# Kernel optimization log

Measured on AMD Instinct MI355X. Metric: run time of the kernel, lower is better.

## Reference

```python
import jax, jax.numpy as jnp
import numpy as np

IN_FEATURES = 4096
OUT_FEATURES = 4096
BLOCK_SIZE = 64
P = 0.1          # fraction of blocks kept
N_TOKENS = 8192


def setup_inputs() -> dict:
    key = jax.random.key(0)
    k_x, k_w, k_m, k_b = jax.random.split(key, 4)
    x = jax.random.normal(k_x, (N_TOKENS, IN_FEATURES), dtype=jnp.float32)
    # kaiming_uniform_(a=sqrt(5)) on [out, in] -> bound = 1/sqrt(in_features)
    bound = 1.0 / np.sqrt(IN_FEATURES)
    weight = jax.random.uniform(k_w, (OUT_FEATURES, IN_FEATURES), dtype=jnp.float32,
                                minval=-bound, maxval=bound)
    bias = jax.random.uniform(k_b, (OUT_FEATURES,), dtype=jnp.float32,
                              minval=-bound, maxval=bound)
    # Block-structured 0/1 mask: keep each BLOCK_SIZE x BLOCK_SIZE block with prob P
    nb_out, nb_in = OUT_FEATURES // BLOCK_SIZE, IN_FEATURES // BLOCK_SIZE
    block_keep = (jax.random.uniform(k_m, (nb_out, nb_in)) < P).astype(jnp.float32)
    mask = jnp.repeat(jnp.repeat(block_keep, BLOCK_SIZE, axis=0), BLOCK_SIZE, axis=1)
    return {"input": x, "weight": weight, "bias": bias, "mask": mask}


def reference(input, weight, bias, mask):
    # bsr_dense_mm((W*mask).to_sparse_bsr(), x.T).T + bias == x @ (W*mask).T + bias
    masked_w = weight * mask                      # [out, in]
    return input @ masked_w.T + bias              # [N, out]
```

## Files before the change

### kernel.cpp

```cpp
#include <hip/hip_runtime.h>
#include <hip/hip_fp16.h>
#include <cstdint>

#define IN_F   4096
#define OUT_F  4096
#define BS     64
#define NB     64
#define N_TOK  8192
#define TM     256
#define NMT    (N_TOK / TM)

typedef __attribute__((ext_vector_type(8))) _Float16       f16x8;
typedef __attribute__((ext_vector_type(8))) unsigned short u16x8;
typedef __attribute__((ext_vector_type(4))) unsigned short u16x4;
typedef __attribute__((ext_vector_type(4))) float          f32x4;

#define WS_X16_OFF     0ull
#define WS_X16_BYTES   ((size_t)N_TOK * IN_F * 2ull)
#define WS_WT_OFF      (WS_X16_OFF + WS_X16_BYTES)
#define WS_WT_BYTES    (4096ull * 8192ull)
#define WS_NEEDED      (WS_WT_OFF + WS_WT_BYTES)

__device__ __forceinline__ unsigned long long mask_ballot(
        const float* __restrict__ mask, int br, int lane) {
    float mv = mask[(size_t)(br * BS) * IN_F + (size_t)lane * BS];
    return __ballot(mv != 0.0f);
}

__device__ __forceinline__ u16x8 pack8(f32x4 a, f32x4 b) {
    u16x8 o;
#pragma unroll
    for (int j = 0; j < 4; ++j) o[j]     = __half_as_ushort(__float2half_rn(a[j]));
#pragma unroll
    for (int j = 0; j < 4; ++j) o[4 + j] = __half_as_ushort(__float2half_rn(b[j]));
    return o;
}

__global__ __launch_bounds__(256)
void convert_all_kernel(const float* __restrict__ x,
                        const float* __restrict__ w,
                        const float* __restrict__ mask,
                        unsigned short* __restrict__ x16,
                        unsigned short* __restrict__ wt) {
    const int b = blockIdx.x;
    if (b < 4096) {
        const f32x4* xin = (const f32x4*)x;
        u16x4* xo = (u16x4*)x16;
        const size_t base = (size_t)b * 2048 + threadIdx.x;
#pragma unroll
        for (int it = 0; it < 8; ++it) {
            f32x4 v = xin[base + it * 256];
            u16x4 o;
#pragma unroll
            for (int j = 0; j < 4; ++j) o[j] = __half_as_ushort(__float2half_rn(v[j]));
            xo[base + it * 256] = o;
        }
    } else {
        const int wb   = b - 4096;
        const int br   = wb >> 6, si = wb & 63;
        const int lane = threadIdx.x & 63;
        unsigned long long ball = mask_ballot(mask, br, lane);
        if (si >= __popcll(ball)) return;
        bool fl = ((ball >> lane) & 1ull) &&
                  (__popcll(ball & ((1ull << lane) - 1ull)) == si);
        unsigned long long m2 = __ballot(fl);
        const int kb = __ffsll(m2) - 1;
        unsigned short* tile = wt + (size_t)(br * NB + si) * 4096;

        f32x4 va[2], vb[2];
#pragma unroll
        for (int l = 0; l < 2; ++l) {
            int g   = threadIdx.x + l * 256;
            int row = g >> 3, slot = g & 7;
            const f32x4* src = (const f32x4*)(w + (size_t)(br * BS + row) * IN_F
                                              + kb * BS + slot * 8);
            va[l] = src[0];
            vb[l] = src[1];
        }
#pragma unroll
        for (int l = 0; l < 2; ++l) {
            int g   = threadIdx.x + l * 256;
            int row = g >> 3, slot = g & 7;
            *(u16x8*)&tile[row * 64 + ((slot ^ (row & 7)) << 3)] = pack8(va[l], vb[l]);
        }
    }
}

__device__ __forceinline__ void gll16(const void* g, void* l) {
    __builtin_amdgcn_global_load_lds(
        (const __attribute__((address_space(1))) unsigned int*)g,
        (__attribute__((address_space(3))) unsigned int*)l, 16, 0, 0);
}

__global__ __launch_bounds__(256, 2)
void bsr_mfma6_kernel(const unsigned short* __restrict__ x16,
                      const unsigned short* __restrict__ wt,
                      const float* __restrict__ bias,
                      const float* __restrict__ mask,
                      float* __restrict__ out) {
    __shared__ unsigned short xs[2][TM * BS];
    __shared__ unsigned short wsb[2][BS * BS];

    const int b     = blockIdx.x;
    const int xcd   = b & 7;
    const int j     = b >> 3;
    const int phase = j >> 7;
    const int idx   = j & 127;
    const int br    = idx >> 1;
    const int mt    = xcd * 4 + phase * 2 + (idx & 1);

    const int tid  = threadIdx.x;
    const int lane = tid & 63;
    const int wv   = tid >> 6;
    const int fr   = lane & 15;
    const int kg   = lane >> 4;

    unsigned long long ball = mask_ballot(mask, br, lane);
    const int cnt = __popcll(ball);

    f32x4 acc[4][4];
#pragma unroll
    for (int a = 0; a < 4; ++a)
#pragma unroll
        for (int c = 0; c < 4; ++c) acc[a][c] = (f32x4)0.0f;

    int preA[8];
#pragma unroll
    for (int q = 0; q < 8; ++q) {
        int rl = wv * 64 + q * 8 + (lane >> 3);
        int s  = (lane & 7) ^ (rl & 7);
        preA[q] = rl * (IN_F * 2) + s * 16;
    }

    const char* xslab = (const char*)x16 + (size_t)(mt * TM) * (IN_F * 2);
    const char* wbase = (const char*)wt;

    auto stage = [&](int kb, int si, int bb) {
        const char* xg = xslab + (size_t)kb * 128;
        const char* wg = wbase + ((size_t)(br * 64 + si) << 13);
        char* ldsA = (char*)xs[bb] + wv * 8192;
#pragma unroll
        for (int q = 0; q < 8; ++q)
            gll16(xg + preA[q], ldsA + q * 1024);
        const int bw = wv * 2048;
#pragma unroll
        for (int q = 0; q < 2; ++q)
            gll16(wg + bw + q * 1024 + lane * 16, (char*)wsb[bb] + bw + q * 1024);
    };

    unsigned long long rem = ball;
    int cur = 0;
    if (cnt > 0) {
        int kb0 = __ffsll(rem) - 1;
        rem &= rem - 1;
        stage(kb0, 0, 0);
    }
    __syncthreads();

    for (int si = 0; si < cnt; ++si) {
        if (si + 1 < cnt) {
            int kbn = __ffsll(rem) - 1;
            rem &= rem - 1;
            stage(kbn, si + 1, cur ^ 1);
        }

#pragma unroll
        for (int ks = 0; ks < 2; ++ks) {
            f16x8 a[4], bfr[4];
#pragma unroll
            for (int mr = 0; mr < 4; ++mr) {
                int row = wv * 64 + mr * 16 + fr;
                a[mr] = *(const f16x8*)&xs[cur][row * 64 + (((ks * 4 + kg) ^ (row & 7)) << 3)];
            }
#pragma unroll
            for (int nr = 0; nr < 4; ++nr) {
                int row = nr * 16 + fr;
                bfr[nr] = *(const f16x8*)&wsb[cur][row * 64 + (((ks * 4 + kg) ^ (row & 7)) << 3)];
            }
#pragma unroll
            for (int mr = 0; mr < 4; ++mr)
#pragma unroll
                for (int nr = 0; nr < 4; ++nr)
                    acc[mr][nr] = __builtin_amdgcn_mfma_f32_16x16x32_f16(
                        a[mr], bfr[nr], acc[mr][nr], 0, 0, 0);
        }
        __syncthreads();
        cur ^= 1;
    }

    const int mbase = mt * TM;
    const int obase = br * BS;
#pragma unroll
    for (int nr = 0; nr < 4; ++nr) {
        float bv = bias[obase + nr * 16 + fr];
#pragma unroll
        for (int mr = 0; mr < 4; ++mr) {
#pragma unroll
            for (int r = 0; r < 4; ++r) {
                int m = mbase + wv * 64 + mr * 16 + kg * 4 + r;
                out[(size_t)m * OUT_F + obase + nr * 16 + fr] = acc[mr][nr][r] + bv;
            }
        }
    }
}

__global__ __launch_bounds__(256, 3)
void bsr_fused_kernel(const float* __restrict__ x,
                      const float* __restrict__ w,
                      const float* __restrict__ bias,
                      const float* __restrict__ mask,
                      float* __restrict__ out) {
    __shared__ unsigned short xs[128 * BS];
    __shared__ unsigned short wsb[BS * BS];

    const int mt   = blockIdx.x;
    const int br   = blockIdx.y;
    const int tid  = threadIdx.x;
    const int lane = tid & 63;
    const int wv   = tid >> 6;
    const int fr   = lane & 15;
    const int kg   = lane >> 4;

    const int mbase = mt * 128;
    const int obase = br * BS;

    unsigned long long ball = mask_ballot(mask, br, lane);
    const int cnt = __popcll(ball);
    unsigned long long rem = ball;

    f32x4 acc[2][4];
#pragma unroll
    for (int a = 0; a < 2; ++a)
#pragma unroll
        for (int c = 0; c < 4; ++c) acc[a][c] = (f32x4)0.0f;

    for (int si = 0; si < cnt; ++si) {
        const int kb = __ffsll(rem) - 1;
        rem &= rem - 1;
        const int kbase = kb * BS;
#pragma unroll
        for (int l = 0; l < 4; ++l) {
            int g = tid + l * 256;
            int row = g >> 3, slot = g & 7;
            const f32x4* src = (const f32x4*)(x + (size_t)(mbase + row) * IN_F + kbase + slot * 8);
            *(u16x8*)&xs[row * BS + ((slot ^ (row & 7)) << 3)] = pack8(src[0], src[1]);
        }
#pragma unroll
        for (int l = 0; l < 2; ++l) {
            int g = tid + l * 256;
            int row = g >> 3, slot = g & 7;
            const f32x4* src = (const f32x4*)(w + (size_t)(obase + row) * IN_F + kbase + slot * 8);
            *(u16x8*)&wsb[row * BS + ((slot ^ (row & 7)) << 3)] = pack8(src[0], src[1]);
        }
        __syncthreads();
#pragma unroll
        for (int ks = 0; ks < 2; ++ks) {
            f16x8 a[2], bfr[4];
#pragma unroll
            for (int mr = 0; mr < 2; ++mr) {
                int row = wv * 32 + mr * 16 + fr;
                a[mr] = *(const f16x8*)&xs[row * BS + (((ks * 4 + kg) ^ (row & 7)) << 3)];
            }
#pragma unroll
            for (int nr = 0; nr < 4; ++nr) {
                int row = nr * 16 + fr;
                bfr[nr] = *(const f16x8*)&wsb[row * BS + (((ks * 4 + kg) ^ (row & 7)) << 3)];
            }
#pragma unroll
            for (int mr = 0; mr < 2; ++mr)
#pragma unroll
                for (int nr = 0; nr < 4; ++nr)
                    acc[mr][nr] = __builtin_amdgcn_mfma_f32_16x16x32_f16(
                        a[mr], bfr[nr], acc[mr][nr], 0, 0, 0);
        }
        __syncthreads();
    }

#pragma unroll
    for (int nr = 0; nr < 4; ++nr) {
        float bv = bias[obase + nr * 16 + fr];
#pragma unroll
        for (int mr = 0; mr < 2; ++mr) {
#pragma unroll
            for (int r = 0; r < 4; ++r) {
                int m = mbase + wv * 32 + mr * 16 + kg * 4 + r;
                out[(size_t)m * OUT_F + obase + nr * 16 + fr] = acc[mr][nr][r] + bv;
            }
        }
    }
}

extern "C" void kernel_launch(void* const* d_in, const int* in_sizes, int n_in,
                              void* d_out, int out_size, void* d_ws, size_t ws_size,
                              hipStream_t stream) {
    const float* x    = (const float*)d_in[0];
    const float* w    = (const float*)d_in[1];
    const float* bias = (const float*)d_in[2];
    const float* mask = (const float*)d_in[3];
    float* out = (float*)d_out;

    if (ws_size >= WS_NEEDED) {
        unsigned short* x16 = (unsigned short*)((char*)d_ws + WS_X16_OFF);
        unsigned short* wt  = (unsigned short*)((char*)d_ws + WS_WT_OFF);
        convert_all_kernel<<<8192, 256, 0, stream>>>(x, w, mask, x16, wt);
        bsr_mfma6_kernel<<<NMT * NB, 256, 0, stream>>>(x16, wt, bias, mask, out);
    } else {
        dim3 grid(N_TOK / 128, NB);
        bsr_fused_kernel<<<grid, 256, 0, stream>>>(x, w, bias, mask, out);
    }
}
```

Before: 110.4 us.

## Pre-tile fp16 activations into contiguous swizzled 256x64 tiles for the GEMM

The conversion kernel now writes x as fp16 tiles of 256 rows by 64 columns. Each tile is contiguous in memory and carries the same XOR swizzle the GEMM expects in LDS. It builds these tiles by staging rows through shared memory. The GEMM's global-to-LDS loads for x become fully linear 16-byte-per-lane copies instead of 128-byte row segments spread across rows, which should cut address math and give better coalescing and cache-line use. In exchange the conversion pass uses fewer, heavier blocks with shared-memory transposes and two barriers per iteration, which may lengthen the preprocessing step.

```diff
diff --git a/kernel.cpp b/kernel.cpp
--- a/kernel.cpp
+++ b/kernel.cpp
@@ -15,9 +15,9 @@
 typedef __attribute__((ext_vector_type(4))) unsigned short u16x4;
 typedef __attribute__((ext_vector_type(4))) float          f32x4;
 
-#define WS_X16_OFF     0ull
-#define WS_X16_BYTES   ((size_t)N_TOK * IN_F * 2ull)
-#define WS_WT_OFF      (WS_X16_OFF + WS_X16_BYTES)
+#define WS_XT_OFF      0ull
+#define WS_XT_BYTES    (2048ull * 32768ull)
+#define WS_WT_OFF      (WS_XT_OFF + WS_XT_BYTES)
 #define WS_WT_BYTES    (4096ull * 8192ull)
 #define WS_NEEDED      (WS_WT_OFF + WS_WT_BYTES)
 
@@ -36,27 +36,49 @@
     return o;
 }
 
-__global__ __launch_bounds__(256)
+__global__ __launch_bounds__(256, 2)
 void convert_all_kernel(const float* __restrict__ x,
                         const float* __restrict__ w,
                         const float* __restrict__ mask,
-                        unsigned short* __restrict__ x16,
+                        unsigned short* __restrict__ xt,
                         unsigned short* __restrict__ wt) {
     const int b = blockIdx.x;
-    if (b < 4096) {
-        const f32x4* xin = (const f32x4*)x;
-        u16x4* xo = (u16x4*)x16;
-        const size_t base = (size_t)b * 2048 + threadIdx.x;
-#pragma unroll
-        for (int it = 0; it < 8; ++it) {
-            f32x4 v = xin[base + it * 256];
-            u16x4 o;
-#pragma unroll
-            for (int j = 0; j < 4; ++j) o[j] = __half_as_ushort(__float2half_rn(v[j]));
-            xo[base + it * 256] = o;
+    if (b < 1024) {
+        __shared__ unsigned short tlds[8][8][64];
+        const int mt = b >> 5;
+        const int rb = b & 31;
+        const int t  = threadIdx.x;
+        const size_t xrow0 = (size_t)(mt * TM + rb * 8) * IN_F;
+        unsigned short* tb = xt + (size_t)(mt * 64) * 16384;
+
+        for (int j = 0; j < 8; ++j) {
+#pragma unroll
+            for (int l = 0; l < 4; ++l) {
+                int id = l * 256 + t;
+                int r  = id >> 7, c4 = id & 127;
+                f32x4 v = *(const f32x4*)(x + xrow0 + (size_t)r * IN_F
+                                          + j * 512 + c4 * 4);
+                u16x4 o;
+#pragma unroll
+                for (int k = 0; k < 4; ++k) o[k] = __half_as_ushort(__float2half_rn(v[k]));
+                int kbl = c4 >> 4, c4k = c4 & 15;
+                int slot = c4k >> 1, h0 = (c4k & 1) * 4;
+                *(u16x4*)&tlds[kbl][r][((slot ^ r) << 3) + h0] = o;
+            }
+            __syncthreads();
+#pragma unroll
+            for (int l = 0; l < 2; ++l) {
+                int wid = l * 256 + t;
+                int kk = wid >> 6, e = wid & 63;
+                int row = e >> 3, s8 = e & 7;
+                u16x8 v = *(const u16x8*)&tlds[kk][row][s8 * 8];
+                unsigned short* tile = tb + (size_t)(j * 8 + kk) * 16384;
+                *(u16x8*)&tile[(rb * 8 + row) * 64 + s8 * 8] = v;
+            }
+            __syncthreads();
         }
     } else {
-        const int wb   = b - 4096;
+        const int wb   = b - 1024;
         const int br   = wb >> 6, si = wb & 63;
         const int lane = threadIdx.x & 63;
         unsigned long long ball = mask_ballot(mask, br, lane);
@@ -93,7 +115,7 @@
 }
 
 __global__ __launch_bounds__(256, 2)
-void bsr_mfma6_kernel(const unsigned short* __restrict__ x16,
+void bsr_mfma5_kernel(const unsigned short* __restrict__ xt,
                       const unsigned short* __restrict__ wt,
                       const float* __restrict__ bias,
                       const float* __restrict__ mask,
@@ -124,24 +146,16 @@
 #pragma unroll
         for (int c = 0; c < 4; ++c) acc[a][c] = (f32x4)0.0f;
 
-    int preA[8];
-#pragma unroll
-    for (int q = 0; q < 8; ++q) {
-        int rl = wv * 64 + q * 8 + (lane >> 3);
-        int s  = (lane & 7) ^ (rl & 7);
-        preA[q] = rl * (IN_F * 2) + s * 16;
-    }
-
-    const char* xslab = (const char*)x16 + (size_t)(mt * TM) * (IN_F * 2);
+    const char* xbase = (const char*)xt;
     const char* wbase = (const char*)wt;
 
     auto stage = [&](int kb, int si, int bb) {
-        const char* xg = xslab + (size_t)kb * 128;
+        const char* xg = xbase + ((size_t)(mt * 64 + kb) << 15);
         const char* wg = wbase + ((size_t)(br * 64 + si) << 13);
-        char* ldsA = (char*)xs[bb] + wv * 8192;
+        const int bx = wv * 8192;
 #pragma unroll
         for (int q = 0; q < 8; ++q)
-            gll16(xg + preA[q], ldsA + q * 1024);
+            gll16(xg + bx + q * 1024 + lane * 16, (char*)xs[bb] + bx + q * 1024);
         const int bw = wv * 2048;
 #pragma unroll
         for (int q = 0; q < 2; ++q)
@@ -300,10 +314,10 @@
     float* out = (float*)d_out;
 
     if (ws_size >= WS_NEEDED) {
-        unsigned short* x16 = (unsigned short*)((char*)d_ws + WS_X16_OFF);
-        unsigned short* wt  = (unsigned short*)((char*)d_ws + WS_WT_OFF);
-        convert_all_kernel<<<8192, 256, 0, stream>>>(x, w, mask, x16, wt);
-        bsr_mfma6_kernel<<<NMT * NB, 256, 0, stream>>>(x16, wt, bias, mask, out);
+        unsigned short* xt = (unsigned short*)((char*)d_ws + WS_XT_OFF);
+        unsigned short* wt = (unsigned short*)((char*)d_ws + WS_WT_OFF);
+        convert_all_kernel<<<1024 + NB * NB, 256, 0, stream>>>(x, w, mask, xt, wt);
+        bsr_mfma5_kernel<<<NMT * NB, 256, 0, stream>>>(xt, wt, bias, mask, out);
     } else {
         dim3 grid(N_TOK / 128, NB);
         bsr_fused_kernel<<<grid, 256, 0, stream>>>(x, w, bias, mask, out);
```

Result: no change. 112.1 us (+1.6%).

## Pre-swizzle x16 during conversion and stage A tiles through registers

Applied to the files above, without the earlier changes.

The fp32-to-fp16 conversion now writes x in an already XOR-swizzled column order, so each 64-column block is stored in the layout the LDS tile expects. The GEMM kernel then replaces the per-lane scattered global_load_lds for the A tile with contiguous 16-byte register loads. These are issued before the MFMA work and written to the other LDS buffer after it, overlapping global latency with compute. This costs 32 extra VGPRs per thread for the register staging, which may pressure occupancy at two blocks per SM.

```diff
diff --git a/kernel.cpp b/kernel.cpp
--- a/kernel.cpp
+++ b/kernel.cpp
@@ -44,16 +44,19 @@
                         unsigned short* __restrict__ wt) {
     const int b = blockIdx.x;
     if (b < 4096) {
-        const f32x4* xin = (const f32x4*)x;
         u16x4* xo = (u16x4*)x16;
-        const size_t base = (size_t)b * 2048 + threadIdx.x;
 #pragma unroll
         for (int it = 0; it < 8; ++it) {
-            f32x4 v = xin[base + it * 256];
+            const size_t f = (size_t)b * 2048 + it * 256 + threadIdx.x;
+            const int row = (int)(f >> 10);
+            const int c   = (int)(f & 1023);
+            const int kb  = c >> 4, sl = (c >> 1) & 7, h = c & 1;
+            const int sc4 = (kb << 4) + (((sl ^ (row & 7)) << 1) + h);
+            f32x4 v = *(const f32x4*)(x + (size_t)row * IN_F + sc4 * 4);
             u16x4 o;
 #pragma unroll
             for (int j = 0; j < 4; ++j) o[j] = __half_as_ushort(__float2half_rn(v[j]));
-            xo[base + it * 256] = o;
+            xo[f] = o;
         }
     } else {
         const int wb   = b - 4096;
@@ -93,7 +96,7 @@
 }
 
 __global__ __launch_bounds__(256, 2)
-void bsr_mfma6_kernel(const unsigned short* __restrict__ x16,
+void bsr_mfma7_kernel(const unsigned short* __restrict__ x16,
                       const unsigned short* __restrict__ wt,
                       const float* __restrict__ bias,
                       const float* __restrict__ mask,
@@ -124,24 +127,25 @@
 #pragma unroll
         for (int c = 0; c < 4; ++c) acc[a][c] = (f32x4)0.0f;
 
-    int preA[8];
-#pragma unroll
-    for (int q = 0; q < 8; ++q) {
-        int rl = wv * 64 + q * 8 + (lane >> 3);
-        int s  = (lane & 7) ^ (rl & 7);
-        preA[q] = rl * (IN_F * 2) + s * 16;
-    }
-
-    const char* xslab = (const char*)x16 + (size_t)(mt * TM) * (IN_F * 2);
+    const int rl_lane = lane >> 3;
+    const int seg     = lane & 7;
+    const unsigned short* xsl = x16 + (size_t)(mt * TM + wv * 64) * IN_F;
     const char* wbase = (const char*)wt;
 
-    auto stage = [&](int kb, int si, int bb) {
-        const char* xg = xslab + (size_t)kb * 128;
+    u16x8 rA[8];
+    auto loadA = [&](int kb) {
+#pragma unroll
+        for (int q = 0; q < 8; ++q)
+            rA[q] = *(const u16x8*)&xsl[(size_t)(q * 8 + rl_lane) * IN_F
+                                        + kb * 64 + seg * 8];
+    };
+    auto writeA = [&](int bb) {
+#pragma unroll
+        for (int q = 0; q < 8; ++q)
+            *(u16x8*)&xs[bb][(wv * 64 + q * 8 + rl_lane) * 64 + seg * 8] = rA[q];
+    };
+    auto stageW = [&](int si, int bb) {
         const char* wg = wbase + ((size_t)(br * 64 + si) << 13);
-        char* ldsA = (char*)xs[bb] + wv * 8192;
-#pragma unroll
-        for (int q = 0; q < 8; ++q)
-            gll16(xg + preA[q], ldsA + q * 1024);
         const int bw = wv * 2048;
 #pragma unroll
         for (int q = 0; q < 2; ++q)
@@ -153,15 +157,19 @@
     if (cnt > 0) {
         int kb0 = __ffsll(rem) - 1;
         rem &= rem - 1;
-        stage(kb0, 0, 0);
+        loadA(kb0);
+        stageW(0, 0);
+        writeA(0);
     }
     __syncthreads();
 
     for (int si = 0; si < cnt; ++si) {
-        if (si + 1 < cnt) {
+        const bool more = (si + 1 < cnt);
+        if (more) {
             int kbn = __ffsll(rem) - 1;
             rem &= rem - 1;
-            stage(kbn, si + 1, cur ^ 1);
+            loadA(kbn);
+            stageW(si + 1, cur ^ 1);
         }
 
 #pragma unroll
@@ -184,6 +192,7 @@
                     acc[mr][nr] = __builtin_amdgcn_mfma_f32_16x16x32_f16(
                         a[mr], bfr[nr], acc[mr][nr], 0, 0, 0);
         }
+        if (more) writeA(cur ^ 1);
         __syncthreads();
         cur ^= 1;
     }
@@ -303,7 +312,7 @@
         unsigned short* x16 = (unsigned short*)((char*)d_ws + WS_X16_OFF);
         unsigned short* wt  = (unsigned short*)((char*)d_ws + WS_WT_OFF);
         convert_all_kernel<<<8192, 256, 0, stream>>>(x, w, mask, x16, wt);
-        bsr_mfma6_kernel<<<NMT * NB, 256, 0, stream>>>(x16, wt, bias, mask, out);
+        bsr_mfma7_kernel<<<NMT * NB, 256, 0, stream>>>(x16, wt, bias, mask, out);
     } else {
         dim3 grid(N_TOK / 128, NB);
         bsr_fused_kernel<<<grid, 256, 0, stream>>>(x, w, bias, mask, out);
```

Result: slower. 112.8 us (+2.2%).
